# Kernel tuning notes

Hardware: AMD Instinct MI355X
Metric: run time of the kernel (lower is better)

## Reference

```python
import jax, jax.numpy as jnp
import numpy as np

B, S, E = 4, 4096, 1024
H = 16
D = E // H            # per-head dim (k_dim == v_dim == 64)
N_SAMPLE = 1024       # tokens kept per (batch, head)


def setup_inputs() -> dict:
    key = jax.random.key(0)
    ks = jax.random.split(key, 7)
    lim = float(np.sqrt(6.0 / (E + E)))  # xavier_uniform for square weight
    x = jax.random.normal(ks[0], (B, S, E), dtype=jnp.float32)
    Wq = jax.random.uniform(ks[1], (E, E), jnp.float32, -lim, lim)
    Wk = jax.random.uniform(ks[2], (E, E), jnp.float32, -lim, lim)
    Wv = jax.random.uniform(ks[3], (E, E), jnp.float32, -lim, lim)
    bq = jnp.zeros((E,), jnp.float32)
    bk = jnp.zeros((E,), jnp.float32)
    bv = jnp.zeros((E,), jnp.float32)
    return {"x": x, "Wq": Wq, "bq": bq, "Wk": Wk, "bk": bk, "Wv": Wv, "bv": bv}


def reference(x, Wq, bq, Wk, bk, Wv, bv):
    Bs, Sl, Ed = x.shape
    # projections -> [B, H, S, D]
    q = (x @ Wq.T + bq).reshape(Bs, Sl, H, D).transpose(0, 2, 1, 3)
    k = (x @ Wk.T + bk).reshape(Bs, Sl, H, D).transpose(0, 2, 1, 3)
    v = (x @ Wv.T + bv).reshape(Bs, Sl, H, D).transpose(0, 2, 1, 3)

    # cosFormer feature map: relu + cos/sin positional reweighting
    pos = jnp.arange(Sl, dtype=x.dtype)
    theta = (jnp.pi / 2.0) * pos / Sl            # [S]
    cos_w = jnp.cos(theta)[None, None, :, None]  # [1,1,S,1]
    sin_w = jnp.sin(theta)[None, None, :, None]
    qn = jax.nn.relu(q)
    kn = jax.nn.relu(k)
    q_cos, q_sin = qn * cos_w, qn * sin_w
    k_cos, k_sin = kn * cos_w, kn * sin_w

    # token sampler: top-N_SAMPLE tokens by (q*k).sum(-1) per (b,h)
    scores = jnp.sum(q * k, axis=-1)             # [B,H,S]
    _, idx = jax.lax.top_k(scores, N_SAMPLE)     # [B,H,n]

    # global K^T V reductions: [B,H,D,D]
    kv_cos = jnp.einsum("bhsd,bhse->bhde", k_cos, v)
    kv_sin = jnp.einsum("bhsd,bhse->bhde", k_sin, v)

    # gather sampled queries: [B,H,n,D]
    qs_cos = jnp.take_along_axis(q_cos, idx[..., None], axis=2)
    qs_sin = jnp.take_along_axis(q_sin, idx[..., None], axis=2)

    sampled = (jnp.einsum("bhnd,bhde->bhne", qs_cos, kv_cos)
               + jnp.einsum("bhnd,bhde->bhne", qs_sin, kv_sin))  # [B,H,n,D]

    # scatter-add back into zeros at sampled positions
    bi = jnp.arange(Bs)[:, None, None]
    hi = jnp.arange(H)[None, :, None]
    values = jnp.zeros((Bs, H, Sl, D), sampled.dtype).at[bi, hi, idx].add(sampled)

    out = values.transpose(0, 2, 1, 3).reshape(Bs, Sl, H * D)
    return out  # o_proj is Identity (v_dim*num_heads == embed_dim); dropout=0
```

## Files before the change

kernel.cpp:

```cpp
#include <hip/hip_runtime.h>
#include <hip/hip_bf16.h>

#define B_ 4
#define S_ 4096
#define E_ 1024
#define H_ 16
#define D_ 64
#define NS_ 1024
#define M_ (B_*S_)
#define K_ E_
#define DELTA 0.12f
#define BANDCAP 96

typedef __attribute__((ext_vector_type(8))) short bf16x8;
typedef __attribute__((ext_vector_type(4))) float floatx4;

#define THSTEP 0.00038349519697141023f

__device__ inline float bf16_to_f(unsigned short u) {
    return __uint_as_float(((unsigned)u) << 16);
}
__device__ inline unsigned short f_to_bf16(float f) {
    unsigned u = __float_as_uint(f);
    unsigned r = (u + 0x7FFFu + ((u >> 16) & 1u)) >> 16;
    return (unsigned short)r;
}

__device__ inline void gl_lds16(const void* g, void* l) {
    __builtin_amdgcn_global_load_lds(
        (const __attribute__((address_space(1))) void*)g,
        (__attribute__((address_space(3))) void*)l, 16, 0, 0);
}

__global__ __launch_bounds__(256) void split_x_kernel(
    const float* __restrict__ x, ushort* __restrict__ xh)
{
    int i = blockIdx.x * 256 + threadIdx.x;
    float4 v = ((const float4*)x)[i];
    ushort4 hh;
    hh.x = f_to_bf16(v.x); hh.y = f_to_bf16(v.y);
    hh.z = f_to_bf16(v.z); hh.w = f_to_bf16(v.w);
    ((ushort4*)xh)[i] = hh;
}

__global__ __launch_bounds__(256) void split_w_kernel(
    const float* __restrict__ Wq, const float* __restrict__ Wk,
    const float* __restrict__ Wv,
    ushort* __restrict__ Wqh, ushort* __restrict__ Wql,
    ushort* __restrict__ Wkh, ushort* __restrict__ Wkl,
    ushort* __restrict__ Wvh)
{
    int i = blockIdx.x * 256 + threadIdx.x;
    float4 q = ((const float4*)Wq)[i];
    float4 k = ((const float4*)Wk)[i];
    float4 v = ((const float4*)Wv)[i];
    ushort4 h, l;
    h.x=f_to_bf16(q.x); l.x=f_to_bf16(q.x-bf16_to_f(h.x));
    h.y=f_to_bf16(q.y); l.y=f_to_bf16(q.y-bf16_to_f(h.y));
    h.z=f_to_bf16(q.z); l.z=f_to_bf16(q.z-bf16_to_f(h.z));
    h.w=f_to_bf16(q.w); l.w=f_to_bf16(q.w-bf16_to_f(h.w));
    ((ushort4*)Wqh)[i]=h; ((ushort4*)Wql)[i]=l;
    h.x=f_to_bf16(k.x); l.x=f_to_bf16(k.x-bf16_to_f(h.x));
    h.y=f_to_bf16(k.y); l.y=f_to_bf16(k.y-bf16_to_f(h.y));
    h.z=f_to_bf16(k.z); l.z=f_to_bf16(k.z-bf16_to_f(h.z));
    h.w=f_to_bf16(k.w); l.w=f_to_bf16(k.w-bf16_to_f(h.w));
    ((ushort4*)Wkh)[i]=h; ((ushort4*)Wkl)[i]=l;
    h.x=f_to_bf16(v.x); h.y=f_to_bf16(v.y);
    h.z=f_to_bf16(v.z); h.w=f_to_bf16(v.w);
    ((ushort4*)Wvh)[i]=h;
}

__global__ __launch_bounds__(256) void qkv_gemm(
    const ushort* __restrict__ xh,
    const ushort* __restrict__ Wqh, const ushort* __restrict__ Wql,
    const ushort* __restrict__ Wkh, const ushort* __restrict__ Wkl,
    const ushort* __restrict__ Wvh,
    const float* __restrict__ bq, const float* __restrict__ bk,
    const float* __restrict__ bv,
    float* __restrict__ q32, float* __restrict__ k32, ushort* __restrict__ v16)
{
    __shared__ __align__(16) ushort As[128 * 64];
    __shared__ __align__(16) ushort Bsh[128 * 64];
    __shared__ __align__(16) ushort Bsl[128 * 64];

    const int w = blockIdx.z;
    const ushort* Bhp = (w == 0) ? Wqh : (w == 1) ? Wkh : Wvh;
    const ushort* Blp = (w == 0) ? Wql : Wkl;
    const float* bias = (w == 0) ? bq : (w == 1) ? bk : bv;
    const bool lo = (w < 2);

    const int m0 = blockIdx.x * 128;
    const int n0 = blockIdx.y * 128;
    const int t = threadIdx.x;
    const int wave = t >> 6, lane = t & 63;
    const int wm = (wave >> 1) * 64, wn = (wave & 1) * 64;
    const int m16 = lane & 15, quad = lane >> 4;

    floatx4 acc[4][4];
#pragma unroll
    for (int i = 0; i < 4; i++)
#pragma unroll
        for (int j = 0; j < 4; j++) acc[i][j] = (floatx4){0.f, 0.f, 0.f, 0.f};

    int aoff[4], boff[4], lbase[4];
#pragma unroll
    for (int i = 0; i < 4; i++) {
        int slot = i * 256 + t;
        int r = slot >> 3, c = slot & 7, g = c ^ (r & 7);
        aoff[i] = (m0 + r) * K_ + g * 8;
        boff[i] = (n0 + r) * K_ + g * 8;
        lbase[i] = (i * 256 + wave * 64) * 8;
    }

    for (int ks = 0; ks < 16; ++ks) {
        const int kcol = ks * 64;
#pragma unroll
        for (int i = 0; i < 4; i++) {
            gl_lds16(xh + aoff[i] + kcol, &As[lbase[i]]);
            gl_lds16(Bhp + boff[i] + kcol, &Bsh[lbase[i]]);
        }
        if (lo) {
#pragma unroll
            for (int i = 0; i < 4; i++)
                gl_lds16(Blp + boff[i] + kcol, &Bsl[lbase[i]]);
        }
        __syncthreads();

#pragma unroll
        for (int kk = 0; kk < 2; ++kk) {
            bf16x8 af[4], bfr[4];
            const int g = kk * 4 + quad;
#pragma unroll
            for (int mt = 0; mt < 4; ++mt) {
                int r = wm + mt * 16 + m16;
                af[mt] = *(const bf16x8*)&As[(r * 8 + (g ^ (r & 7))) * 8];
            }
#pragma unroll
            for (int nt = 0; nt < 4; ++nt) {
                int r2 = wn + nt * 16 + m16;
                bfr[nt] = *(const bf16x8*)&Bsh[(r2 * 8 + (g ^ (r2 & 7))) * 8];
            }
#pragma unroll
            for (int mt = 0; mt < 4; ++mt)
#pragma unroll
                for (int nt = 0; nt < 4; ++nt)
                    acc[mt][nt] = __builtin_amdgcn_mfma_f32_16x16x32_bf16(
                        af[mt], bfr[nt], acc[mt][nt], 0, 0, 0);
            if (lo) {
#pragma unroll
                for (int nt = 0; nt < 4; ++nt) {
                    int r2 = wn + nt * 16 + m16;
                    bfr[nt] = *(const bf16x8*)&Bsl[(r2 * 8 + (g ^ (r2 & 7))) * 8];
                }
#pragma unroll
                for (int mt = 0; mt < 4; ++mt)
#pragma unroll
                    for (int nt = 0; nt < 4; ++nt)
                        acc[mt][nt] = __builtin_amdgcn_mfma_f32_16x16x32_bf16(
                            af[mt], bfr[nt], acc[mt][nt], 0, 0, 0);
            }
        }
        __syncthreads();
    }

    float biasv[4];
#pragma unroll
    for (int nt = 0; nt < 4; nt++)
        biasv[nt] = bias[n0 + wn + nt * 16 + m16];

    if (w < 2) {
        float* dst = (w == 0) ? q32 : k32;
#pragma unroll
        for (int mt = 0; mt < 4; ++mt)
#pragma unroll
            for (int nt = 0; nt < 4; ++nt) {
                int colg = n0 + wn + nt * 16 + m16;
#pragma unroll
                for (int reg = 0; reg < 4; ++reg) {
                    int rowg = m0 + wm + mt * 16 + quad * 4 + reg;
                    dst[(size_t)rowg * E_ + colg] = acc[mt][nt][reg] + biasv[nt];
                }
            }
    } else {
#pragma unroll
        for (int mt = 0; mt < 4; ++mt)
#pragma unroll
            for (int nt = 0; nt < 4; ++nt) {
                int colg = n0 + wn + nt * 16 + m16;
#pragma unroll
                for (int reg = 0; reg < 4; ++reg) {
                    int rowg = m0 + wm + mt * 16 + quad * 4 + reg;
                    v16[(size_t)rowg * E_ + colg] = f_to_bf16(acc[mt][nt][reg] + biasv[nt]);
                }
            }
    }
}

__global__ __launch_bounds__(256) void scores_kernel(
    const float* __restrict__ q32, const float* __restrict__ k32,
    float* __restrict__ scores)
{
    int wid = blockIdx.x * 4 + (threadIdx.x >> 6);
    int lane = threadIdx.x & 63;
    int s = wid & (S_ - 1);
    int bh = wid >> 12;
    int b = bh >> 4, h = bh & 15;
    size_t addr = (size_t)(b * S_ + s) * E_ + h * 64 + lane;
    float p = q32[addr] * k32[addr];
#pragma unroll
    for (int m = 32; m; m >>= 1) p += __shfl_xor(p, m, 64);
    if (lane == 0) scores[wid] = p;
}

__global__ __launch_bounds__(256) void band_select_kernel(
    const float* __restrict__ scores, int* __restrict__ selidx,
    int* __restrict__ band, int* __restrict__ meta)
{
    __shared__ unsigned keys[4096];
    __shared__ unsigned hist[256];
    __shared__ unsigned suf[256];
    __shared__ unsigned bcast[2];
    __shared__ int cnt_in, cnt_band;

    int bh = blockIdx.x;
    int t = threadIdx.x;
    const float* sc = scores + (size_t)bh * S_;

    for (int i = t; i < 4096; i += 256) {
        unsigned u = __float_as_uint(sc[i]);
        u = (u & 0x80000000u) ? ~u : (u | 0x80000000u);
        keys[i] = u;
    }
    if (t == 0) { cnt_in = 0; cnt_band = 0; }
    __syncthreads();

    unsigned prefix = 0, want = NS_;
    for (int shift = 24; shift >= 0; shift -= 8) {
        hist[t] = 0;
        __syncthreads();
        unsigned pmask = (shift == 24) ? 0u : (0xFFFFFFFFu << (shift + 8));
        for (int i = t; i < 4096; i += 256) {
            unsigned ky = keys[i];
            if ((ky & pmask) == prefix) atomicAdd(&hist[(ky >> shift) & 255u], 1u);
        }
        __syncthreads();
        suf[t] = hist[t];
        __syncthreads();
        for (int off = 1; off < 256; off <<= 1) {
            unsigned add = (t + off < 256) ? suf[t + off] : 0u;
            __syncthreads();
            suf[t] += add;
            __syncthreads();
        }
        unsigned Sb = suf[t];
        unsigned Snx = (t < 255) ? suf[t + 1] : 0u;
        if (Sb >= want && Snx < want) {
            bcast[0] = (unsigned)t;
            bcast[1] = want - Snx;
        }
        __syncthreads();
        prefix = prefix | (bcast[0] << shift);
        want = bcast[1];
        __syncthreads();
    }
    unsigned fb = (prefix & 0x80000000u) ? (prefix ^ 0x80000000u) : ~prefix;
    float Ta = __uint_as_float(fb);
    float Thi = Ta + DELTA, Tlo = Ta - DELTA;

    int* sel = selidx + (size_t)bh * NS_;
    int* bnd = band + (size_t)bh * BANDCAP;
    for (int i = t; i < 4096; i += 256) {
        float v = sc[i];
        if (v > Thi) {
            int p = atomicAdd(&cnt_in, 1);
            sel[p] = i;
        } else if (v >= Tlo) {
            int p = atomicAdd(&cnt_band, 1);
            if (p < BANDCAP) bnd[p] = i;
        }
    }
    __syncthreads();
    if (t == 0) {
        meta[bh * 2 + 0] = cnt_in;
        meta[bh * 2 + 1] = (cnt_band < BANDCAP) ? cnt_band : BANDCAP;
    }
}

__global__ __launch_bounds__(512) void band_exact_kernel(
    const float* __restrict__ x,
    const float* __restrict__ Wq, const float* __restrict__ Wk,
    const int* __restrict__ band, const int* __restrict__ meta,
    double* __restrict__ bscore)
{
    int j = blockIdx.x, bh = blockIdx.y;
    int NB = meta[bh * 2 + 1];
    if (j >= NB) return;
    int b = bh >> 4, h = bh & 15;
    int s = band[(size_t)bh * BANDCAP + j];
    int t = threadIdx.x;
    int wave = t >> 6, lane = t & 63;

    __shared__ float xs[1024];
    __shared__ double qkd[128];

    if (t < 256)
        *(float4*)&xs[t * 4] = *(const float4*)(x + (size_t)(b * S_ + s) * K_ + t * 4);
    __syncthreads();

    const float* Wbase = (wave < 4) ? Wq : Wk;
    int role = wave >> 2;
    int dbase = (wave & 3) * 16;
    const float4* xs4 = (const float4*)xs;

    for (int rr = 0; rr < 16; ++rr) {
        int d = dbase + rr;
        const float4* wrow4 = (const float4*)(Wbase + (size_t)(h * 64 + d) * K_);
        double a = 0.0;
#pragma unroll
        for (int p = 0; p < 4; ++p) {
            float4 wv = wrow4[lane + 64 * p];
            float4 xv = xs4[lane + 64 * p];
            a += (double)xv.x * wv.x + (double)xv.y * wv.y
               + (double)xv.z * wv.z + (double)xv.w * wv.w;
        }
#pragma unroll
        for (int m = 32; m; m >>= 1) a += __shfl_xor(a, m, 64);
        if (lane == 0) qkd[role * 64 + d] = a;
    }
    __syncthreads();

    if (t < 64) {
        double p = qkd[t] * qkd[64 + t];
#pragma unroll
        for (int m = 32; m; m >>= 1) p += __shfl_xor(p, m, 64);
        if (t == 0) bscore[(size_t)bh * BANDCAP + j] = p;
    }
}

__global__ __launch_bounds__(128) void band_rank_kernel(
    const double* __restrict__ bscore, const int* __restrict__ band,
    const int* __restrict__ meta, int* __restrict__ selidx)
{
    __shared__ double sc[BANDCAP];
    __shared__ int bi[BANDCAP];
    int bh = blockIdx.x, t = threadIdx.x;
    int cnt_in = meta[bh * 2 + 0], NB = meta[bh * 2 + 1];
    int need = NS_ - cnt_in;
    if (t < NB) {
        sc[t] = bscore[(size_t)bh * BANDCAP + t];
        bi[t] = band[(size_t)bh * BANDCAP + t];
    }
    __syncthreads();
    if (t < NB) {
        double mine = sc[t]; int myi = bi[t]; int r = 0;
        for (int j2 = 0; j2 < NB; ++j2)
            r += (sc[j2] > mine) || (sc[j2] == mine && bi[j2] < myi);
        if (r < need) selidx[(size_t)bh * NS_ + cnt_in + r] = myi;
    }
}

__global__ __launch_bounds__(256) void kv_mfma_kernel(
    const float* __restrict__ k32, const ushort* __restrict__ v16,
    float* __restrict__ kvp)
{
    __shared__ __align__(16) ushort P[5 * 64 * 88];

    const int ch = blockIdx.x;
    const int bh = blockIdx.y;
    const int b = bh >> 4, h = bh & 15;
    const int t = threadIdx.x;
    const int wave = t >> 6, lane = t & 63;
    const int m16 = lane & 15, quad = lane >> 4;
    const int wm = (wave >> 1) * 32, wn = (wave & 1) * 32;
    const int d0 = wave * 16;

    const float*  kbase = k32 + (size_t)b * S_ * E_ + h * 64 + d0;
    const ushort* vbase = v16 + (size_t)b * S_ * E_ + h * 64 + d0;

    floatx4 acc[2][2][2];
#pragma unroll
    for (int p = 0; p < 2; p++)
#pragma unroll
        for (int i = 0; i < 2; i++)
#pragma unroll
            for (int j = 0; j < 2; j++) acc[p][i][j] = (floatx4){0.f,0.f,0.f,0.f};

    float  ka[16];
    ushort va[16];
    int sg = ch * 256 + lane;
    {
        const float*  kr = kbase + (size_t)sg * E_;
        const ushort* vr = vbase + (size_t)sg * E_;
#pragma unroll
        for (int j = 0; j < 4; ++j) *(float4*)&ka[j * 4] = ((const float4*)kr)[j];
        *(uint4*)&va[0] = *(const uint4*)vr;
        *(uint4*)&va[8] = *(const uint4*)(vr + 8);
    }

    for (int grp = 0; grp < 4; ++grp) {
        float th = (float)sg * THSTEP;
        float cw = __cosf(th), sw = __sinf(th);
        int s_loc = lane;

        __syncthreads();
#pragma unroll
        for (int j = 0; j < 16; ++j) {
            float kr_ = fmaxf(ka[j], 0.f);
            float pc = kr_ * cw, ps = kr_ * sw;
            ushort chh = f_to_bf16(pc);
            ushort cll = f_to_bf16(pc - bf16_to_f(chh));
            ushort shh = f_to_bf16(ps);
            ushort sll = f_to_bf16(ps - bf16_to_f(shh));
            int r = (d0 + j) * 88 + s_loc;
            P[0 * 5632 + r] = chh;
            P[1 * 5632 + r] = cll;
            P[2 * 5632 + r] = shh;
            P[3 * 5632 + r] = sll;
            P[4 * 5632 + r] = va[j];
        }
        __syncthreads();

        if (grp < 3) {
            sg += 64;
            const float*  kr = kbase + (size_t)sg * E_;
            const ushort* vr = vbase + (size_t)sg * E_;
#pragma unroll
            for (int j = 0; j < 4; ++j) *(float4*)&ka[j * 4] = ((const float4*)kr)[j];
            *(uint4*)&va[0] = *(const uint4*)vr;
            *(uint4*)&va[8] = *(const uint4*)(vr + 8);
        }

#pragma unroll
        for (int kk = 0; kk < 2; ++kk) {
            const int so = kk * 32 + quad * 8;
            bf16x8 ach[2], acl[2], ash[2], asl[2], bv[2];
#pragma unroll
            for (int mt = 0; mt < 2; ++mt) {
                int r = (wm + mt * 16 + m16) * 88 + so;
                ach[mt] = *(const bf16x8*)&P[0 * 5632 + r];
                acl[mt] = *(const bf16x8*)&P[1 * 5632 + r];
                ash[mt] = *(const bf16x8*)&P[2 * 5632 + r];
                asl[mt] = *(const bf16x8*)&P[3 * 5632 + r];
            }
#pragma unroll
            for (int nt = 0; nt < 2; ++nt) {
                int r = (wn + nt * 16 + m16) * 88 + so;
                bv[nt] = *(const bf16x8*)&P[4 * 5632 + r];
            }
#pragma unroll
            for (int mt = 0; mt < 2; ++mt)
#pragma unroll
                for (int nt = 0; nt < 2; ++nt) {
                    acc[0][mt][nt] = __builtin_amdgcn_mfma_f32_16x16x32_bf16(
                        ach[mt], bv[nt], acc[0][mt][nt], 0, 0, 0);
                    acc[0][mt][nt] = __builtin_amdgcn_mfma_f32_16x16x32_bf16(
                        acl[mt], bv[nt], acc[0][mt][nt], 0, 0, 0);
                    acc[1][mt][nt] = __builtin_amdgcn_mfma_f32_16x16x32_bf16(
                        ash[mt], bv[nt], acc[1][mt][nt], 0, 0, 0);
                    acc[1][mt][nt] = __builtin_amdgcn_mfma_f32_16x16x32_bf16(
                        asl[mt], bv[nt], acc[1][mt][nt], 0, 0, 0);
                }
        }
    }

    float* base = kvp + ((size_t)(bh * 16 + ch) * 2) * 4096;
#pragma unroll
    for (int p = 0; p < 2; ++p)
#pragma unroll
        for (int mt = 0; mt < 2; ++mt)
#pragma unroll
            for (int nt = 0; nt < 2; ++nt)
#pragma unroll
                for (int reg = 0; reg < 4; ++reg) {
                    int row = wm + mt * 16 + quad * 4 + reg;
                    int col = wn + nt * 16 + m16;
                    base[p * 4096 + row * 64 + col] = acc[p][mt][nt][reg];
                }
}

__global__ __launch_bounds__(256) void kv_reduce_kernel(
    const float* __restrict__ kvp, float* __restrict__ kv)
{
    int i = blockIdx.x * 256 + threadIdx.x;
    if (i >= 64 * 2 * 4096) return;
    int bh = i >> 13;
    int rem = i & 8191;
    const float* p = kvp + (size_t)bh * 16 * 8192 + rem;
    float a = 0.f;
#pragma unroll
    for (int c = 0; c < 16; c++) a += p[c * 8192];
    kv[i] = a;
}

__global__ __launch_bounds__(256) void sampled_kernel(
    const float* __restrict__ q32, const int* __restrict__ selidx,
    const float* __restrict__ kv, float* __restrict__ out)
{
    __shared__ float kvc[4096];
    __shared__ float kvs[4096];
    __shared__ float qs[256 * 65];
    __shared__ int sidx[256];
    int bh = blockIdx.y;
    int b = bh >> 4, h = bh & 15;
    int t = threadIdx.x;
    int wave = t >> 6, lane = t & 63;

    const float* kvsrc = kv + (size_t)bh * 8192;
    for (int i = t; i < 4096; i += 256) {
        kvc[i] = kvsrc[i];
        kvs[i] = kvsrc[4096 + i];
    }
    sidx[t] = selidx[(size_t)bh * NS_ + blockIdx.x * 256 + t];
    __syncthreads();

    for (int i = 0; i < 64; ++i) {
        int row = wave * 64 + i;
        int sr = sidx[row];
        qs[row * 65 + lane] = q32[(size_t)(b * S_ + sr) * E_ + h * 64 + lane];
    }
    __syncthreads();

    int s = sidx[t];
    float th = (float)s * THSTEP;
    float cw = __cosf(th), sw = __sinf(th);

    float acc[64];
#pragma unroll
    for (int e = 0; e < 64; e++) acc[e] = 0.f;

    for (int d = 0; d < 64; ++d) {
        float qd = fmaxf(qs[t * 65 + d], 0.f);
        float a = qd * cw, bb = qd * sw;
        const float4* pc4 = (const float4*)&kvc[d * 64];
        const float4* ps4 = (const float4*)&kvs[d * 64];
#pragma unroll
        for (int e4 = 0; e4 < 16; e4++) {
            float4 c4 = pc4[e4], s4 = ps4[e4];
            acc[e4 * 4 + 0] += a * c4.x + bb * s4.x;
            acc[e4 * 4 + 1] += a * c4.y + bb * s4.y;
            acc[e4 * 4 + 2] += a * c4.z + bb * s4.z;
            acc[e4 * 4 + 3] += a * c4.w + bb * s4.w;
        }
    }
    __syncthreads();
#pragma unroll
    for (int e = 0; e < 64; e++) qs[t * 65 + e] = acc[e];
    __syncthreads();

    for (int i = 0; i < 64; ++i) {
        int row = wave * 64 + i;
        int sr = sidx[row];
        out[(size_t)(b * S_ + sr) * E_ + h * 64 + lane] = qs[row * 65 + lane];
    }
}

__global__ void zero_kernel(uint4* __restrict__ p, int n16)
{
    int stride = gridDim.x * blockDim.x;
    for (int i = blockIdx.x * blockDim.x + threadIdx.x; i < n16; i += stride)
        p[i] = make_uint4(0u, 0u, 0u, 0u);
}

extern "C" void kernel_launch(void* const* d_in, const int* in_sizes, int n_in,
                              void* d_out, int out_size, void* d_ws, size_t ws_size,
                              hipStream_t stream)
{
    const float* x  = (const float*)d_in[0];
    const float* Wq = (const float*)d_in[1];
    const float* bq = (const float*)d_in[2];
    const float* Wk = (const float*)d_in[3];
    const float* bk = (const float*)d_in[4];
    const float* Wv = (const float*)d_in[5];
    const float* bv = (const float*)d_in[6];

    char* ws = (char*)d_ws;
    ushort* xh     = (ushort*)(ws);
    float*  kvp    = (float*)(ws);
    float*  q32    = (float*)(ws + 33554432);
    float*  k32    = (float*)(ws + 100663296);
    ushort* v16    = (ushort*)(ws + 167772160);
    ushort* Wqh    = (ushort*)(ws + 201326592);
    ushort* Wql    = (ushort*)(ws + 203423744);
    ushort* Wkh    = (ushort*)(ws + 205520896);
    ushort* Wkl    = (ushort*)(ws + 207618048);
    ushort* Wvh    = (ushort*)(ws + 209715200);
    float*  scores = (float*)(ws + 211812352);
    int*    selidx = (int*)(ws + 212860928);
    int*    band   = (int*)(ws + 213123072);
    double* bscore = (double*)(ws + 213147648);
    int*    meta   = (int*)(ws + 213196800);
    float*  kv     = (float*)(ws + 213197312);
    float*  out    = (float*)d_out;

    hipLaunchKernelGGL(zero_kernel, dim3(2048), dim3(256), 0, stream,
                       (uint4*)out, (int)((size_t)M_ * E_ * 4 / 16));
    hipLaunchKernelGGL(split_x_kernel, dim3((M_ * K_) / 1024), dim3(256), 0, stream,
                       x, xh);
    hipLaunchKernelGGL(split_w_kernel, dim3((E_ * E_) / 1024), dim3(256), 0, stream,
                       Wq, Wk, Wv, Wqh, Wql, Wkh, Wkl, Wvh);
    hipLaunchKernelGGL(qkv_gemm, dim3(128, 8, 3), dim3(256), 0, stream,
                       xh, Wqh, Wql, Wkh, Wkl, Wvh, bq, bk, bv, q32, k32, v16);
    hipLaunchKernelGGL(scores_kernel, dim3((B_ * H_ * S_) / 4), dim3(256), 0, stream,
                       q32, k32, scores);
    hipLaunchKernelGGL(band_select_kernel, dim3(B_ * H_), dim3(256), 0, stream,
                       scores, selidx, band, meta);
    hipLaunchKernelGGL(band_exact_kernel, dim3(BANDCAP, B_ * H_), dim3(512), 0, stream,
                       x, Wq, Wk, band, meta, bscore);
    hipLaunchKernelGGL(band_rank_kernel, dim3(B_ * H_), dim3(128), 0, stream,
                       bscore, band, meta, selidx);
    hipLaunchKernelGGL(kv_mfma_kernel, dim3(16, 64), dim3(256), 0, stream,
                       k32, v16, kvp);
    hipLaunchKernelGGL(kv_reduce_kernel, dim3(2048), dim3(256), 0, stream,
                       kvp, kv);
    hipLaunchKernelGGL(sampled_kernel, dim3(NS_ / 256, B_ * H_), dim3(256), 0, stream,
                       q32, selidx, kv, out);
}
```

Before: 509.8 us.

## Fuse prep kernels, vectorize scores, wave-scan radix select, retile sampled kernel

Merges the output zeroing, x bf16 conversion and weight hi/lo splitting into one prep kernel, cutting launches. The scores kernel now uses 16 lanes with float4 loads per token. Band select replaces the LDS suffix scan, with its many barriers, by wave shuffles. The exact-score dot product gets split double accumulators. The sampled kernel moves from 256 tokens per block with 64 accumulators per thread to 64 tokens with 4 threads per token, packed float2 math and direct float4 stores, which lowers register pressure and raises parallelism.

```diff
diff --git a/kernel.cpp b/kernel.cpp
--- a/kernel.cpp
+++ b/kernel.cpp
@@ -14,6 +14,7 @@
 
 typedef __attribute__((ext_vector_type(8))) short bf16x8;
 typedef __attribute__((ext_vector_type(4))) float floatx4;
+typedef __attribute__((ext_vector_type(2))) float f32x2;
 
 #define THSTEP 0.00038349519697141023f
 
@@ -32,42 +33,50 @@
         (__attribute__((address_space(3))) void*)l, 16, 0, 0);
 }
 
-__global__ __launch_bounds__(256) void split_x_kernel(
-    const float* __restrict__ x, ushort* __restrict__ xh)
-{
-    int i = blockIdx.x * 256 + threadIdx.x;
-    float4 v = ((const float4*)x)[i];
-    ushort4 hh;
-    hh.x = f_to_bf16(v.x); hh.y = f_to_bf16(v.y);
-    hh.z = f_to_bf16(v.z); hh.w = f_to_bf16(v.w);
-    ((ushort4*)xh)[i] = hh;
-}
-
-__global__ __launch_bounds__(256) void split_w_kernel(
+__global__ __launch_bounds__(256) void prep_kernel(
+    const float* __restrict__ x,
     const float* __restrict__ Wq, const float* __restrict__ Wk,
     const float* __restrict__ Wv,
+    ushort* __restrict__ xh,
     ushort* __restrict__ Wqh, ushort* __restrict__ Wql,
     ushort* __restrict__ Wkh, ushort* __restrict__ Wkl,
-    ushort* __restrict__ Wvh)
-{
-    int i = blockIdx.x * 256 + threadIdx.x;
-    float4 q = ((const float4*)Wq)[i];
-    float4 k = ((const float4*)Wk)[i];
-    float4 v = ((const float4*)Wv)[i];
-    ushort4 h, l;
-    h.x=f_to_bf16(q.x); l.x=f_to_bf16(q.x-bf16_to_f(h.x));
-    h.y=f_to_bf16(q.y); l.y=f_to_bf16(q.y-bf16_to_f(h.y));
-    h.z=f_to_bf16(q.z); l.z=f_to_bf16(q.z-bf16_to_f(h.z));
-    h.w=f_to_bf16(q.w); l.w=f_to_bf16(q.w-bf16_to_f(h.w));
-    ((ushort4*)Wqh)[i]=h; ((ushort4*)Wql)[i]=l;
-    h.x=f_to_bf16(k.x); l.x=f_to_bf16(k.x-bf16_to_f(h.x));
-    h.y=f_to_bf16(k.y); l.y=f_to_bf16(k.y-bf16_to_f(h.y));
-    h.z=f_to_bf16(k.z); l.z=f_to_bf16(k.z-bf16_to_f(h.z));
-    h.w=f_to_bf16(k.w); l.w=f_to_bf16(k.w-bf16_to_f(h.w));
-    ((ushort4*)Wkh)[i]=h; ((ushort4*)Wkl)[i]=l;
-    h.x=f_to_bf16(v.x); h.y=f_to_bf16(v.y);
-    h.z=f_to_bf16(v.z); h.w=f_to_bf16(v.w);
-    ((ushort4*)Wvh)[i]=h;
+    ushort* __restrict__ Wvh,
+    uint4* __restrict__ outz)
+{
+    int t = blockIdx.x * 256 + threadIdx.x;
+    uint4 z = make_uint4(0u, 0u, 0u, 0u);
+#pragma unroll
+    for (int c = 0; c < 4; ++c)
+        outz[c * 1048576 + t] = z;
+#pragma unroll
+    for (int c = 0; c < 4; ++c) {
+        int i = c * 1048576 + t;
+        float4 v = ((const float4*)x)[i];
+        ushort4 hh;
+        hh.x = f_to_bf16(v.x); hh.y = f_to_bf16(v.y);
+        hh.z = f_to_bf16(v.z); hh.w = f_to_bf16(v.w);
+        ((ushort4*)xh)[i] = hh;
+    }
+    if (t < 262144) {
+        int i = t;
+        float4 q = ((const float4*)Wq)[i];
+        float4 k = ((const float4*)Wk)[i];
+        float4 v = ((const float4*)Wv)[i];
+        ushort4 h, l;
+        h.x=f_to_bf16(q.x); l.x=f_to_bf16(q.x-bf16_to_f(h.x));
+        h.y=f_to_bf16(q.y); l.y=f_to_bf16(q.y-bf16_to_f(h.y));
+        h.z=f_to_bf16(q.z); l.z=f_to_bf16(q.z-bf16_to_f(h.z));
+        h.w=f_to_bf16(q.w); l.w=f_to_bf16(q.w-bf16_to_f(h.w));
+        ((ushort4*)Wqh)[i]=h; ((ushort4*)Wql)[i]=l;
+        h.x=f_to_bf16(k.x); l.x=f_to_bf16(k.x-bf16_to_f(h.x));
+        h.y=f_to_bf16(k.y); l.y=f_to_bf16(k.y-bf16_to_f(h.y));
+        h.z=f_to_bf16(k.z); l.z=f_to_bf16(k.z-bf16_to_f(h.z));
+        h.w=f_to_bf16(k.w); l.w=f_to_bf16(k.w-bf16_to_f(h.w));
+        ((ushort4*)Wkh)[i]=h; ((ushort4*)Wkl)[i]=l;
+        h.x=f_to_bf16(v.x); h.y=f_to_bf16(v.y);
+        h.z=f_to_bf16(v.z); h.w=f_to_bf16(v.w);
+        ((ushort4*)Wvh)[i]=h;
+    }
 }
 
 __global__ __launch_bounds__(256) void qkv_gemm(
@@ -200,16 +209,18 @@
     const float* __restrict__ q32, const float* __restrict__ k32,
     float* __restrict__ scores)
 {
-    int wid = blockIdx.x * 4 + (threadIdx.x >> 6);
-    int lane = threadIdx.x & 63;
-    int s = wid & (S_ - 1);
-    int bh = wid >> 12;
+    int g = blockIdx.x * 16 + (threadIdx.x >> 4);
+    int sub = threadIdx.x & 15;
+    int s = g & (S_ - 1);
+    int bh = g >> 12;
     int b = bh >> 4, h = bh & 15;
-    size_t addr = (size_t)(b * S_ + s) * E_ + h * 64 + lane;
-    float p = q32[addr] * k32[addr];
-#pragma unroll
-    for (int m = 32; m; m >>= 1) p += __shfl_xor(p, m, 64);
-    if (lane == 0) scores[wid] = p;
+    size_t addr = (size_t)(b * S_ + s) * E_ + h * 64 + sub * 4;
+    float4 qv = *(const float4*)(q32 + addr);
+    float4 kv = *(const float4*)(k32 + addr);
+    float p = qv.x * kv.x + qv.y * kv.y + qv.z * kv.z + qv.w * kv.w;
+#pragma unroll
+    for (int m = 8; m; m >>= 1) p += __shfl_xor(p, m, 64);
+    if (sub == 0) scores[g] = p;
 }
 
 __global__ __launch_bounds__(256) void band_select_kernel(
@@ -218,12 +229,13 @@
 {
     __shared__ unsigned keys[4096];
     __shared__ unsigned hist[256];
-    __shared__ unsigned suf[256];
+    __shared__ unsigned wtot[4];
     __shared__ unsigned bcast[2];
     __shared__ int cnt_in, cnt_band;
 
     int bh = blockIdx.x;
     int t = threadIdx.x;
+    int wave = t >> 6, lane = t & 63;
     const float* sc = scores + (size_t)bh * S_;
 
     for (int i = t; i < 4096; i += 256) {
@@ -232,7 +244,6 @@
         keys[i] = u;
     }
     if (t == 0) { cnt_in = 0; cnt_band = 0; }
-    __syncthreads();
 
     unsigned prefix = 0, want = NS_;
     for (int shift = 24; shift >= 0; shift -= 8) {
@@ -244,16 +255,21 @@
             if ((ky & pmask) == prefix) atomicAdd(&hist[(ky >> shift) & 255u], 1u);
         }
         __syncthreads();
-        suf[t] = hist[t];
-        __syncthreads();
-        for (int off = 1; off < 256; off <<= 1) {
-            unsigned add = (t + off < 256) ? suf[t + off] : 0u;
-            __syncthreads();
-            suf[t] += add;
-            __syncthreads();
-        }
-        unsigned Sb = suf[t];
-        unsigned Snx = (t < 255) ? suf[t + 1] : 0u;
+        unsigned sv = hist[t];
+#pragma unroll
+        for (int off = 1; off < 64; off <<= 1) {
+            unsigned o = __shfl_down(sv, off, 64);
+            sv += (lane + off < 64) ? o : 0u;
+        }
+        if (lane == 0) wtot[wave] = sv;
+        __syncthreads();
+        unsigned cross = 0;
+#pragma unroll
+        for (int w2 = 0; w2 < 4; ++w2)
+            cross += (w2 > wave) ? wtot[w2] : 0u;
+        unsigned Sb = sv + cross;
+        unsigned sv1 = __shfl_down(sv, 1, 64);
+        unsigned Snx = (lane < 63) ? sv1 + cross : cross;
         if (Sb >= want && Snx < want) {
             bcast[0] = (unsigned)t;
             bcast[1] = want - Snx;
@@ -315,14 +331,17 @@
     for (int rr = 0; rr < 16; ++rr) {
         int d = dbase + rr;
         const float4* wrow4 = (const float4*)(Wbase + (size_t)(h * 64 + d) * K_);
-        double a = 0.0;
+        double a0 = 0.0, a1 = 0.0, a2 = 0.0, a3 = 0.0;
 #pragma unroll
         for (int p = 0; p < 4; ++p) {
             float4 wv = wrow4[lane + 64 * p];
             float4 xv = xs4[lane + 64 * p];
-            a += (double)xv.x * wv.x + (double)xv.y * wv.y
-               + (double)xv.z * wv.z + (double)xv.w * wv.w;
-        }
+            a0 += (double)xv.x * wv.x;
+            a1 += (double)xv.y * wv.y;
+            a2 += (double)xv.z * wv.z;
+            a3 += (double)xv.w * wv.w;
+        }
+        double a = (a0 + a1) + (a2 + a3);
 #pragma unroll
         for (int m = 32; m; m >>= 1) a += __shfl_xor(a, m, 64);
         if (lane == 0) qkd[role * 64 + d] = a;
@@ -496,69 +515,68 @@
     const float* __restrict__ q32, const int* __restrict__ selidx,
     const float* __restrict__ kv, float* __restrict__ out)
 {
-    __shared__ float kvc[4096];
-    __shared__ float kvs[4096];
-    __shared__ float qs[256 * 65];
-    __shared__ int sidx[256];
+    __shared__ __align__(16) float kvc[4096];
+    __shared__ __align__(16) float kvs[4096];
+    __shared__ __align__(16) float qs[64 * 68];
+    __shared__ int sidx[64];
     int bh = blockIdx.y;
     int b = bh >> 4, h = bh & 15;
     int t = threadIdx.x;
-    int wave = t >> 6, lane = t & 63;
-
-    const float* kvsrc = kv + (size_t)bh * 8192;
-    for (int i = t; i < 4096; i += 256) {
-        kvc[i] = kvsrc[i];
-        kvs[i] = kvsrc[4096 + i];
-    }
-    sidx[t] = selidx[(size_t)bh * NS_ + blockIdx.x * 256 + t];
+
+    const float4* kvsrc4 = (const float4*)(kv + (size_t)bh * 8192);
+    float4* kvc4 = (float4*)kvc;
+    float4* kvs4 = (float4*)kvs;
+#pragma unroll
+    for (int i = 0; i < 4; ++i) {
+        kvc4[i * 256 + t] = kvsrc4[i * 256 + t];
+        kvs4[i * 256 + t] = kvsrc4[1024 + i * 256 + t];
+    }
+    if (t < 64) sidx[t] = selidx[(size_t)bh * NS_ + blockIdx.x * 64 + t];
     __syncthreads();
 
-    for (int i = 0; i < 64; ++i) {
-        int row = wave * 64 + i;
+#pragma unroll
+    for (int c = 0; c < 4; ++c) {
+        int i = c * 256 + t;
+        int row = i >> 4, qp = i & 15;
         int sr = sidx[row];
-        qs[row * 65 + lane] = q32[(size_t)(b * S_ + sr) * E_ + h * 64 + lane];
+        *(float4*)&qs[row * 68 + qp * 4] =
+            *(const float4*)(q32 + (size_t)(b * S_ + sr) * E_ + h * 64 + qp * 4);
     }
     __syncthreads();
 
-    int s = sidx[t];
-    float th = (float)s * THSTEP;
+    int tok = t >> 2, eq = t & 3;
+    int sr = sidx[tok];
+    float th = (float)sr * THSTEP;
     float cw = __cosf(th), sw = __sinf(th);
 
-    float acc[64];
-#pragma unroll
-    for (int e = 0; e < 64; e++) acc[e] = 0.f;
-
+    f32x2 acc2[8];
+#pragma unroll
+    for (int e = 0; e < 8; e++) acc2[e] = (f32x2){0.f, 0.f};
+
+    const float4* kvcb = (const float4*)&kvc[eq * 16];
+    const float4* kvsb = (const float4*)&kvs[eq * 16];
     for (int d = 0; d < 64; ++d) {
-        float qd = fmaxf(qs[t * 65 + d], 0.f);
-        float a = qd * cw, bb = qd * sw;
-        const float4* pc4 = (const float4*)&kvc[d * 64];
-        const float4* ps4 = (const float4*)&kvs[d * 64];
-#pragma unroll
-        for (int e4 = 0; e4 < 16; e4++) {
-            float4 c4 = pc4[e4], s4 = ps4[e4];
-            acc[e4 * 4 + 0] += a * c4.x + bb * s4.x;
-            acc[e4 * 4 + 1] += a * c4.y + bb * s4.y;
-            acc[e4 * 4 + 2] += a * c4.z + bb * s4.z;
-            acc[e4 * 4 + 3] += a * c4.w + bb * s4.w;
-        }
-    }
-    __syncthreads();
-#pragma unroll
-    for (int e = 0; e < 64; e++) qs[t * 65 + e] = acc[e];
-    __syncthreads();
-
-    for (int i = 0; i < 64; ++i) {
-        int row = wave * 64 + i;
-        int sr = sidx[row];
-        out[(size_t)(b * S_ + sr) * E_ + h * 64 + lane] = qs[row * 65 + lane];
-    }
-}
-
-__global__ void zero_kernel(uint4* __restrict__ p, int n16)
-{
-    int stride = gridDim.x * blockDim.x;
-    for (int i = blockIdx.x * blockDim.x + threadIdx.x; i < n16; i += stride)
-        p[i] = make_uint4(0u, 0u, 0u, 0u);
+        float qd = fmaxf(qs[tok * 68 + d], 0.f);
+        f32x2 a2 = { qd * cw, qd * cw };
+        f32x2 b2 = { qd * sw, qd * sw };
+#pragma unroll
+        for (int c = 0; c < 4; ++c) {
+            float4 c4 = kvcb[d * 16 + c];
+            float4 s4 = kvsb[d * 16 + c];
+            f32x2 c01 = { c4.x, c4.y }, c23 = { c4.z, c4.w };
+            f32x2 s01 = { s4.x, s4.y }, s23 = { s4.z, s4.w };
+            acc2[c * 2 + 0] += a2 * c01 + b2 * s01;
+            acc2[c * 2 + 1] += a2 * c23 + b2 * s23;
+        }
+    }
+
+    float* dst = out + (size_t)(b * S_ + sr) * E_ + h * 64 + eq * 16;
+#pragma unroll
+    for (int c = 0; c < 4; ++c) {
+        float4 o = { acc2[c * 2 + 0][0], acc2[c * 2 + 0][1],
+                     acc2[c * 2 + 1][0], acc2[c * 2 + 1][1] };
+        *(float4*)(dst + c * 4) = o;
+    }
 }
 
 extern "C" void kernel_launch(void* const* d_in, const int* in_sizes, int n_in,
@@ -592,15 +610,11 @@
     float*  kv     = (float*)(ws + 213197312);
     float*  out    = (float*)d_out;
 
-    hipLaunchKernelGGL(zero_kernel, dim3(2048), dim3(256), 0, stream,
-                       (uint4*)out, (int)((size_t)M_ * E_ * 4 / 16));
-    hipLaunchKernelGGL(split_x_kernel, dim3((M_ * K_) / 1024), dim3(256), 0, stream,
-                       x, xh);
-    hipLaunchKernelGGL(split_w_kernel, dim3((E_ * E_) / 1024), dim3(256), 0, stream,
-                       Wq, Wk, Wv, Wqh, Wql, Wkh, Wkl, Wvh);
+    hipLaunchKernelGGL(prep_kernel, dim3(4096), dim3(256), 0, stream,
+                       x, Wq, Wk, Wv, xh, Wqh, Wql, Wkh, Wkl, Wvh, (uint4*)out);
     hipLaunchKernelGGL(qkv_gemm, dim3(128, 8, 3), dim3(256), 0, stream,
                        xh, Wqh, Wql, Wkh, Wkl, Wvh, bq, bk, bv, q32, k32, v16);
-    hipLaunchKernelGGL(scores_kernel, dim3((B_ * H_ * S_) / 4), dim3(256), 0, stream,
+    hipLaunchKernelGGL(scores_kernel, dim3((B_ * H_ * S_) / 16), dim3(256), 0, stream,
                        q32, k32, scores);
     hipLaunchKernelGGL(band_select_kernel, dim3(B_ * H_), dim3(256), 0, stream,
                        scores, selidx, band, meta);
@@ -612,6 +626,6 @@
                        k32, v16, kvp);
     hipLaunchKernelGGL(kv_reduce_kernel, dim3(2048), dim3(256), 0, stream,
                        kvp, kv);
-    hipLaunchKernelGGL(sampled_kernel, dim3(NS_ / 256, B_ * H_), dim3(256), 0, stream,
+    hipLaunchKernelGGL(sampled_kernel, dim3(NS_ / 64, B_ * H_), dim3(256), 0, stream,
                        q32, selidx, kv, out);
 }
```

Measured after the change: 501.6 us. About the same (-1.6%).
